# Kernel tuning notes

Measured on AMD Instinct MI355X. Metric: run time of the kernel, lower is better.

The kernel has to match this reference:

```python
import jax, jax.numpy as jnp
import numpy as np

HIDDEN = 100


def gcn_conv(x, W, b, src, dst, w, n):
    # GCNConv with symmetric normalization (self-loops already appended).
    xw = x @ W                                   # [N, H]
    deg = jax.ops.segment_sum(w, dst, num_segments=n)
    dinv = jnp.where(deg > 0, jax.lax.rsqrt(deg), 0.0)
    norm = dinv[src] * w * dinv[dst]             # [E]
    agg = jax.ops.segment_sum(norm[:, None] * xw[src], dst, num_segments=n)
    return agg + b


def setup_inputs() -> dict:
    key = jax.random.key(0)
    ks = jax.random.split(key, 16)
    N, F, E, H = 100000, 128, 1600000, HIDDEN
    x = jax.random.normal(ks[0], (N, F), dtype=jnp.float32)
    edge_index = jax.random.randint(ks[1], (2, E), 0, N, dtype=jnp.int64)
    edge_weight = jax.random.uniform(ks[2], (E,), dtype=jnp.float32)
    sF = 1.0 / np.sqrt(F)
    sH2 = 1.0 / np.sqrt(2 * H)
    sH = 1.0 / np.sqrt(H)
    inp = {
        "x": x, "edge_index": edge_index, "edge_weight": edge_weight,
        "Wcz": jax.random.normal(ks[3], (F, H), jnp.float32) * sF,
        "bcz": jnp.zeros((H,), jnp.float32),
        "Wcr": jax.random.normal(ks[4], (F, H), jnp.float32) * sF,
        "bcr": jnp.zeros((H,), jnp.float32),
        "Wch": jax.random.normal(ks[5], (F, H), jnp.float32) * sF,
        "bch": jnp.zeros((H,), jnp.float32),
        "Wlz": jax.random.normal(ks[6], (2 * H, H), jnp.float32) * sH2,
        "blz": jnp.zeros((H,), jnp.float32),
        "Wlr": jax.random.normal(ks[7], (2 * H, H), jnp.float32) * sH2,
        "blr": jnp.zeros((H,), jnp.float32),
        "Wlh": jax.random.normal(ks[8], (2 * H, H), jnp.float32) * sH2,
        "blh": jnp.zeros((H,), jnp.float32),
        "Wout": jax.random.normal(ks[9], (H, 1), jnp.float32) * sH,
        "bout": jnp.zeros((1,), jnp.float32),
    }
    return inp


def reference(x, edge_index, edge_weight,
              Wcz, bcz, Wcr, bcr, Wch, bch,
              Wlz, blz, Wlr, blr, Wlh, blh,
              Wout, bout):
    N = x.shape[0]
    # add self-loops with weight 1 (GCNConv default)
    loop = jnp.arange(N, dtype=edge_index.dtype)
    src = jnp.concatenate([edge_index[0], loop])
    dst = jnp.concatenate([edge_index[1], loop])
    w = jnp.concatenate([edge_weight, jnp.ones((N,), edge_weight.dtype)])

    H0 = jnp.zeros((N, HIDDEN), x.dtype)  # TGCN initial hidden state

    cz = gcn_conv(x, Wcz, bcz, src, dst, w, N)
    Z = jax.nn.sigmoid(jnp.concatenate([cz, H0], axis=1) @ Wlz + blz)

    cr = gcn_conv(x, Wcr, bcr, src, dst, w, N)
    R = jax.nn.sigmoid(jnp.concatenate([cr, H0], axis=1) @ Wlr + blr)

    ch = gcn_conv(x, Wch, bch, src, dst, w, N)
    Ht = jnp.tanh(jnp.concatenate([ch, H0 * R], axis=1) @ Wlh + blh)

    Hn = Z * H0 + (1.0 - Z) * Ht
    h = jax.nn.relu(Hn)
    return h @ Wout + bout
```

## Files before the change

kernel.cpp:

```cpp
#include <hip/hip_runtime.h>

#define FEAT 128
#define HID  100
#define CHUNK 2048

typedef __attribute__((ext_vector_type(8))) short short8;
typedef __attribute__((ext_vector_type(4))) float f32x4;

__device__ __forceinline__ unsigned short f2bf(float f) {
    union { float f; unsigned int u; } v; v.f = f;
    unsigned int r = v.u + 0x7fffu + ((v.u >> 16) & 1u);
    return (unsigned short)(r >> 16);
}

__device__ __forceinline__ int get_edge(const void* ei, int f64, long long pos) {
    return f64 ? (int)((const long long*)ei)[pos] : ((const int*)ei)[pos];
}

__device__ __forceinline__ int detect_f64(const void* ei) {
    const int* p = (const int*)ei;
    unsigned long long b = __ballot(p[2 * (threadIdx.x & 63) + 1] == 0);
    return b == ~0ull;
}

__global__ __launch_bounds__(256)
void k_front(const float* __restrict__ x, uint4* __restrict__ xb, int n8,
             const float* __restrict__ Wcz, const float* __restrict__ bcz,
             const float* __restrict__ Wch, const float* __restrict__ bch,
             const float* __restrict__ Wlz, const float* __restrict__ blz,
             const float* __restrict__ Wlh, const float* __restrict__ blh,
             const float* __restrict__ Wout,
             unsigned short* __restrict__ WB, float* __restrict__ bfold_ext,
             float* __restrict__ WoutZ,
             const void* ei, int* __restrict__ bucketCnt,
             int* __restrict__ blockBase, int NB, int E) {
    const int CVTB = 1024, FOLDB = 130;
    __shared__ int hist[1024];
    if (blockIdx.x < CVTB) {
        int stride = CVTB * 256;
        for (int i = blockIdx.x * 256 + threadIdx.x; i < n8; i += stride) {
            float4 a = *(const float4*)(x + (size_t)i * 8);
            float4 b = *(const float4*)(x + (size_t)i * 8 + 4);
            uint4 o;
            o.x = f2bf(a.x) | ((unsigned)f2bf(a.y) << 16);
            o.y = f2bf(a.z) | ((unsigned)f2bf(a.w) << 16);
            o.z = f2bf(b.x) | ((unsigned)f2bf(b.y) << 16);
            o.w = f2bf(b.z) | ((unsigned)f2bf(b.w) << 16);
            xb[i] = o;
        }
        return;
    }
    if (blockIdx.x < CVTB + FOLDB) {
        int idx = (blockIdx.x - CVTB) * 256 + threadIdx.x;
        if (idx < FEAT * 256) {
            int k = idx >> 8, n = idx & 255;
            float val = 0.f;
            if (n < HID) {
                for (int m = 0; m < HID; m++) val += Wcz[k * HID + m] * Wlz[m * HID + n];
            } else if (n >= 128 && n < 128 + HID) {
                int c = n - 128;
                for (int m = 0; m < HID; m++) val += Wch[k * HID + m] * Wlh[m * HID + c];
            }
            int ni = n >> 4, lc = n & 15, ks = k >> 5, hi = (k >> 3) & 3, j = k & 7;
            WB[(((ni * 4 + ks) * 64 + hi * 16 + lc) << 3) + j] = f2bf(val);
        } else if (idx < FEAT * 256 + 256) {
            int c = idx - FEAT * 256;
            float v = 0.f;
            if (c < HID) {
                v = blz[c];
                for (int j = 0; j < HID; j++) v += bcz[j] * Wlz[j * HID + c];
            } else if (c >= 128 && c < 128 + HID) {
                int cc = c - 128;
                v = blh[cc];
                for (int j = 0; j < HID; j++) v += bch[j] * Wlh[j * HID + cc];
            }
            bfold_ext[c] = v;
        } else if (idx < FEAT * 256 + 256 + 128) {
            int c = idx - FEAT * 256 - 256;
            WoutZ[c] = (c < HID) ? Wout[c] : 0.f;
        }
        return;
    }
    int f64 = detect_f64(ei);
    int cb = blockIdx.x - CVTB - FOLDB;
    int t = threadIdx.x;
    for (int i = t; i < NB; i += 256) hist[i] = 0;
    __syncthreads();
    int e0 = cb * CHUNK;
#pragma unroll
    for (int k = 0; k < CHUNK / 256; k++) {
        int e = e0 + k * 256 + t;
        if (e < E) {
            int d = get_edge(ei, f64, (long long)E + e);
            atomicAdd(&hist[d >> 8], 1);
        }
    }
    __syncthreads();
    int* bb = blockBase + (size_t)cb * NB;
    for (int b = t; b < NB; b += 256) {
        int c = hist[b];
        if (c) bb[b] = atomicAdd(&bucketCnt[b], c);
    }
}

__global__ void k_scanb(const int* __restrict__ bucketCnt, int* __restrict__ bucketStart,
                        int NB) {
    __shared__ int lds[1024];
    int t = threadIdx.x;
    int v = (t < NB) ? bucketCnt[t] : 0;
    lds[t] = v;
    __syncthreads();
    for (int off = 1; off < 1024; off <<= 1) {
        int tv = (t >= off) ? lds[t - off] : 0;
        __syncthreads();
        lds[t] += tv;
        __syncthreads();
    }
    if (t < NB) bucketStart[t] = lds[t] - v;
    if (t == NB - 1) bucketStart[NB] = lds[t];
}

__global__ __launch_bounds__(512)
void k_scatter(const void* ei, const float* __restrict__ w,
               const int* __restrict__ bucketStart, const int* __restrict__ blockBase,
               int2* __restrict__ sc, int NB, int E) {
    int f64 = detect_f64(ei);
    __shared__ int hist[1024];
    int t = threadIdx.x;
    for (int i = t; i < NB; i += 512) hist[i] = 0;
    __syncthreads();
    int e0 = blockIdx.x * CHUNK;
    const int* bb = blockBase + (size_t)blockIdx.x * NB;
    int sA[4], dA[4], wA[4], ok[4];
#pragma unroll
    for (int k = 0; k < 4; k++) {
        int e = e0 + k * 512 + t;
        ok[k] = (e < E);
        if (ok[k]) {
            sA[k] = get_edge(ei, f64, e);
            dA[k] = get_edge(ei, f64, (long long)E + e);
            wA[k] = __float_as_int(w[e]);
        }
    }
#pragma unroll
    for (int k = 0; k < 4; k++) {
        if (ok[k]) {
            int b = dA[k] >> 8;
            int r = atomicAdd(&hist[b], 1);
            int pos = bucketStart[b] + bb[b] + r;
            long long val = ((long long)wA[k] << 32)
                          | (unsigned)(sA[k] | ((dA[k] & 255) << 24));
            *(long long*)&sc[pos] = val;
        }
    }
}

__global__ __launch_bounds__(512)
void k_bucket(const int2* __restrict__ sc, const int* __restrict__ bucketStart,
              int* __restrict__ offs, int* __restrict__ cnt,
              int2* __restrict__ csr, float* __restrict__ dinv, int N) {
    __shared__ int hist[256];
    __shared__ int offsL[256];
    __shared__ int rank[256];
    __shared__ float wsum[256];
    int t = threadIdx.x;
    int n0 = blockIdx.x << 8;
    int s = bucketStart[blockIdx.x], e = bucketStart[blockIdx.x + 1];
    if (t < 256) { hist[t] = 0; rank[t] = 0; wsum[t] = 0.f; }
    __syncthreads();
    for (int i = s + t; i < e; i += 512)
        atomicAdd(&hist[((unsigned)sc[i].x) >> 24], 1);
    __syncthreads();
    int v = 0;
    if (t < 256) {
        v = (n0 + t < N) ? hist[t] + 1 : 0;
        offsL[t] = v;
    }
    __syncthreads();
    for (int off = 1; off < 256; off <<= 1) {
        int tv = (t < 256 && t >= off) ? offsL[t - off] : 0;
        __syncthreads();
        if (t < 256) offsL[t] += tv;
        __syncthreads();
    }
    int myOff = 0, myHist = 0;
    if (t < 256) { myOff = offsL[t] - v; myHist = hist[t]; }
    int csrBase = s + n0;
    if (t < 256 && n0 + t < N) {
        offs[n0 + t] = csrBase + myOff;
        cnt[n0 + t] = v;
    }
    __syncthreads();
    if (t < 256) offsL[t] = myOff;
    __syncthreads();
    for (int i = s + t; i < e; i += 512) {
        int2 en = sc[i];
        int dlow = ((unsigned)en.x) >> 24;
        int r = atomicAdd(&rank[dlow], 1);
        csr[csrBase + offsL[dlow] + r] = make_int2(en.x & 0xFFFFFF, en.y);
        atomicAdd(&wsum[dlow], __int_as_float(en.y));
    }
    __syncthreads();
    if (t < 256 && n0 + t < N) {
        dinv[n0 + t] = rsqrtf(1.f + wsum[t]);
        csr[csrBase + myOff + myHist] = make_int2(n0 + t, __float_as_int(1.0f));
    }
}

__global__ __launch_bounds__(256)
void k_agg4(const unsigned short* __restrict__ xb, const float* __restrict__ dinv,
            const int* __restrict__ offs, const int* __restrict__ cnt,
            const int2* __restrict__ csr, unsigned short* __restrict__ aggx,
            int nlo, int nhi) {
    int wid  = __builtin_amdgcn_readfirstlane(threadIdx.x >> 6);
    int lane = threadIdx.x & 63;
    long long node = (long long)nlo + blockIdx.x * 4 + wid;
    if (node >= nhi) return;
    int q  = lane >> 3;
    int fl = lane & 7;
    float acc[16];
#pragma unroll
    for (int j = 0; j < 16; j++) acc[j] = 0.f;
    int rs = offs[node];
    int c  = cnt[node];
    for (int i = q; i < c; i += 8) {
        int2 e = csr[rs + i];
        float nr = __int_as_float(e.y) * dinv[e.x];
        const uint4* xp = (const uint4*)(xb + (size_t)e.x * FEAT + fl * 16);
        uint4 v0 = xp[0];
        uint4 v1 = xp[1];
        const unsigned* u0 = &v0.x;
        const unsigned* u1 = &v1.x;
#pragma unroll
        for (int j = 0; j < 4; j++) {
            acc[2*j]         += nr * __uint_as_float(u0[j] << 16);
            acc[2*j + 1]     += nr * __uint_as_float(u0[j] & 0xffff0000u);
            acc[8 + 2*j]     += nr * __uint_as_float(u1[j] << 16);
            acc[8 + 2*j + 1] += nr * __uint_as_float(u1[j] & 0xffff0000u);
        }
    }
#pragma unroll
    for (int j = 0; j < 16; j++) {
        acc[j] += __shfl_xor(acc[j], 8);
        acc[j] += __shfl_xor(acc[j], 16);
        acc[j] += __shfl_xor(acc[j], 32);
    }
    if (q == 0) {
        float dn = dinv[node];
        uint4 o0, o1;
        unsigned* p0 = &o0.x;
        unsigned* p1 = &o1.x;
#pragma unroll
        for (int j = 0; j < 4; j++) {
            p0[j] = f2bf(acc[2*j] * dn)   | ((unsigned)f2bf(acc[2*j+1] * dn) << 16);
            p1[j] = f2bf(acc[8+2*j] * dn) | ((unsigned)f2bf(acc[8+2*j+1] * dn) << 16);
        }
        uint4* op = (uint4*)(aggx + (size_t)node * FEAT + fl * 16);
        op[0] = o0;
        op[1] = o1;
    }
}

__global__ __launch_bounds__(256)
void k_post3(const unsigned short* __restrict__ aggx, const unsigned short* __restrict__ WB,
             const float* __restrict__ bfold_ext, const float* __restrict__ WoutZ,
             const float* __restrict__ bout, float* __restrict__ out, int N) {
    __shared__ unsigned short At[64 * 136];
    __shared__ float red[64 * 4];
    int t = threadIdx.x;
    int lane = t & 63;
    int w = __builtin_amdgcn_readfirstlane(t >> 6);
    long long base = (long long)blockIdx.x * 64;

    for (int it = 0; it < 4; it++) {
        int idx = it * 256 + t;
        int row = idx >> 4, c16 = idx & 15;
        long long grow = base + row;
        uint4 v = make_uint4(0u, 0u, 0u, 0u);
        if (grow < N) v = *(const uint4*)(aggx + grow * FEAT + c16 * 8);
        *(uint4*)(At + row * 136 + c16 * 8) = v;
    }
    __syncthreads();

    int l15 = lane & 15, lhi = lane >> 4;
    int tadd = 2 * w;
    f32x4 acc[4][4];
#pragma unroll
    for (int ti = 0; ti < 4; ti++)
#pragma unroll
        for (int mi = 0; mi < 4; mi++) acc[ti][mi] = (f32x4)0.f;

    const int tiles[4] = {tadd, tadd + 1, tadd + 8, tadd + 9};
#pragma unroll
    for (int ks = 0; ks < 4; ks++) {
        short8 a[4];
#pragma unroll
        for (int mi = 0; mi < 4; mi++)
            a[mi] = *(const short8*)(At + (mi * 16 + l15) * 136 + ks * 32 + lhi * 8);
        short8 b[4];
#pragma unroll
        for (int ti = 0; ti < 4; ti++)
            b[ti] = *(const short8*)(WB + (((tiles[ti] * 4 + ks) * 64 + lane) << 3));
#pragma unroll
        for (int ti = 0; ti < 4; ti++)
#pragma unroll
            for (int mi = 0; mi < 4; mi++)
                acc[ti][mi] = __builtin_amdgcn_mfma_f32_16x16x32_bf16(
                    a[mi], b[ti], acc[ti][mi], 0, 0, 0);
    }

    float partial[4][4];
#pragma unroll
    for (int mi = 0; mi < 4; mi++)
#pragma unroll
        for (int r = 0; r < 4; r++) partial[mi][r] = 0.f;
#pragma unroll
    for (int d = 0; d < 2; d++) {
        int zcol = (tadd + d) * 16 + l15;
        float bz = bfold_ext[zcol];
        float bh = bfold_ext[zcol + 128];
        float wo = WoutZ[zcol];
#pragma unroll
        for (int mi = 0; mi < 4; mi++)
#pragma unroll
            for (int r = 0; r < 4; r++) {
                float az = acc[d][mi][r] + bz;
                float ah = acc[d + 2][mi][r] + bh;
                float z  = 1.f / (1.f + expf(-az));
                float ht = tanhf(ah);
                float h  = (1.f - z) * ht;
                h = h > 0.f ? h : 0.f;
                partial[mi][r] += h * wo;
            }
    }
#pragma unroll
    for (int mi = 0; mi < 4; mi++)
#pragma unroll
        for (int r = 0; r < 4; r++) {
            float p = partial[mi][r];
            p += __shfl_xor(p, 1);
            p += __shfl_xor(p, 2);
            p += __shfl_xor(p, 4);
            p += __shfl_xor(p, 8);
            partial[mi][r] = p;
        }
    if (l15 == 0) {
#pragma unroll
        for (int mi = 0; mi < 4; mi++)
#pragma unroll
            for (int r = 0; r < 4; r++)
                red[(mi * 16 + lhi * 4 + r) * 4 + w] = partial[mi][r];
    }
    __syncthreads();
    if (t < 64) {
        long long node = base + t;
        if (node < N)
            out[node] = red[t * 4] + red[t * 4 + 1] + red[t * 4 + 2] + red[t * 4 + 3]
                      + bout[0];
    }
}

extern "C" void kernel_launch(void* const* d_in, const int* in_sizes, int n_in,
                              void* d_out, int out_size, void* d_ws, size_t ws_size,
                              hipStream_t stream) {
    const float* x    = (const float*)d_in[0];
    const void*  ei   = d_in[1];
    const float* ew   = (const float*)d_in[2];
    const float* Wcz  = (const float*)d_in[3];
    const float* bcz  = (const float*)d_in[4];
    const float* Wch  = (const float*)d_in[7];
    const float* bch  = (const float*)d_in[8];
    const float* Wlz  = (const float*)d_in[9];
    const float* blz  = (const float*)d_in[10];
    const float* Wlh  = (const float*)d_in[13];
    const float* blh  = (const float*)d_in[14];
    const float* Wout = (const float*)d_in[15];
    const float* bout = (const float*)d_in[16];
    float* out = (float*)d_out;

    int N = in_sizes[0] / FEAT;
    int E = in_sizes[2];
    int NB = (N + 255) >> 8;
    int nblocksA = (E + CHUNK - 1) / CHUNK;

    char* p = (char*)d_ws;
    auto alloc = [&](size_t bytes) -> char* {
        char* r = p;
        p += (bytes + 255) & ~(size_t)255;
        return r;
    };
    float*          dinv        = (float*)alloc((size_t)N * 4);
    int*            cnt         = (int*)  alloc((size_t)N * 4);
    int*            offs        = (int*)  alloc((size_t)N * 4);
    int*            bucketCnt   = (int*)  alloc((size_t)(NB + 1) * 4);
    int*            bucketStart = (int*)  alloc((size_t)(NB + 1) * 4);
    int2*           csr         = (int2*) alloc((size_t)(E + N) * 8);
    unsigned short* xb          = (unsigned short*)alloc((size_t)N * FEAT * 2);
    unsigned short* aggx        = (unsigned short*)alloc((size_t)N * FEAT * 2);
    unsigned short* WB          = (unsigned short*)alloc((size_t)FEAT * 256 * 2);
    float*          bfold_ext   = (float*)alloc(256 * 4);
    float*          WoutZ       = (float*)alloc(128 * 4);
    int2* sc        = (int2*)aggx;
    int*  blockBase = (int*)((char*)aggx + (size_t)E * 8);

    hipMemsetAsync(bucketCnt, 0, (size_t)NB * 4, stream);
    k_front<<<1024 + 130 + nblocksA, 256, 0, stream>>>(
        x, (uint4*)xb, N * FEAT / 8,
        Wcz, bcz, Wch, bch, Wlz, blz, Wlh, blh, Wout, WB, bfold_ext, WoutZ,
        ei, bucketCnt, blockBase, NB, E);
    k_scanb<<<1, 1024, 0, stream>>>(bucketCnt, bucketStart, NB);
    k_scatter<<<nblocksA, 512, 0, stream>>>(ei, ew, bucketStart, blockBase, sc, NB, E);
    k_bucket<<<NB, 512, 0, stream>>>(sc, bucketStart, offs, cnt, csr, dinv, N);
    int Na = 33336, Nb2 = 66668;
    k_agg4<<<(Na + 3) / 4, 256, 0, stream>>>(xb, dinv, offs, cnt, csr, aggx, 0, Na);
    k_agg4<<<(Nb2 - Na + 3) / 4, 256, 0, stream>>>(xb, dinv, offs, cnt, csr, aggx, Na, Nb2);
    k_agg4<<<(N - Nb2 + 3) / 4, 256, 0, stream>>>(xb, dinv, offs, cnt, csr, aggx, Nb2, N);
    k_post3<<<(N + 63) / 64, 256, 0, stream>>>(aggx, WB, bfold_ext, WoutZ, bout, out, N);
}
```

Before: 295.8 us.

## Fuse bucket scan into scatter and bucket kernels, move x conversion, merge agg launches

New measurement: 284.9 us. 3.7% less time.

```diff
diff --git a/kernel.cpp b/kernel.cpp
--- a/kernel.cpp
+++ b/kernel.cpp
@@ -23,9 +23,27 @@
     return b == ~0ull;
 }
 
+__device__ __forceinline__ void scan_buckets(const int* __restrict__ bucketCnt,
+                                             int NB, int* bs) {
+    int t = threadIdx.x;
+    int v = (t < NB) ? bucketCnt[t] : 0;
+    if (t < NB) bs[t] = v;
+    __syncthreads();
+    for (int off = 1; off < NB; off <<= 1) {
+        int tv = (t < NB && t >= off) ? bs[t - off] : 0;
+        __syncthreads();
+        if (t < NB) bs[t] += tv;
+        __syncthreads();
+    }
+    int incl = (t < NB) ? bs[t] : 0;
+    __syncthreads();
+    if (t < NB) bs[t] = incl - v;
+    if (t == NB - 1) bs[NB] = incl;
+    __syncthreads();
+}
+
 __global__ __launch_bounds__(256)
-void k_front(const float* __restrict__ x, uint4* __restrict__ xb, int n8,
-             const float* __restrict__ Wcz, const float* __restrict__ bcz,
+void k_front(const float* __restrict__ Wcz, const float* __restrict__ bcz,
              const float* __restrict__ Wch, const float* __restrict__ bch,
              const float* __restrict__ Wlz, const float* __restrict__ blz,
              const float* __restrict__ Wlh, const float* __restrict__ blh,
@@ -34,24 +52,10 @@
              float* __restrict__ WoutZ,
              const void* ei, int* __restrict__ bucketCnt,
              int* __restrict__ blockBase, int NB, int E) {
-    const int CVTB = 1024, FOLDB = 130;
+    const int FOLDB = 130;
     __shared__ int hist[1024];
-    if (blockIdx.x < CVTB) {
-        int stride = CVTB * 256;
-        for (int i = blockIdx.x * 256 + threadIdx.x; i < n8; i += stride) {
-            float4 a = *(const float4*)(x + (size_t)i * 8);
-            float4 b = *(const float4*)(x + (size_t)i * 8 + 4);
-            uint4 o;
-            o.x = f2bf(a.x) | ((unsigned)f2bf(a.y) << 16);
-            o.y = f2bf(a.z) | ((unsigned)f2bf(a.w) << 16);
-            o.z = f2bf(b.x) | ((unsigned)f2bf(b.y) << 16);
-            o.w = f2bf(b.z) | ((unsigned)f2bf(b.w) << 16);
-            xb[i] = o;
-        }
-        return;
-    }
-    if (blockIdx.x < CVTB + FOLDB) {
-        int idx = (blockIdx.x - CVTB) * 256 + threadIdx.x;
+    if (blockIdx.x < FOLDB) {
+        int idx = blockIdx.x * 256 + threadIdx.x;
         if (idx < FEAT * 256) {
             int k = idx >> 8, n = idx & 255;
             float val = 0.f;
@@ -82,7 +86,7 @@
         return;
     }
     int f64 = detect_f64(ei);
-    int cb = blockIdx.x - CVTB - FOLDB;
+    int cb = blockIdx.x - FOLDB;
     int t = threadIdx.x;
     for (int i = t; i < NB; i += 256) hist[i] = 0;
     __syncthreads();
@@ -103,34 +107,36 @@
     }
 }
 
-__global__ void k_scanb(const int* __restrict__ bucketCnt, int* __restrict__ bucketStart,
-                        int NB) {
-    __shared__ int lds[1024];
+__global__ __launch_bounds__(512)
+void k_scvt(const float* __restrict__ x, uint4* __restrict__ xb, int n8,
+            const void* ei, const float* __restrict__ w,
+            const int* __restrict__ bucketCnt, const int* __restrict__ blockBase,
+            int2* __restrict__ sc, int NB, int E) {
+    const int CVTB = 1024;
+    __shared__ int hist[1024];
+    __shared__ int bs[1024];
+    if (blockIdx.x < CVTB) {
+        int stride = CVTB * 512;
+        for (int i = blockIdx.x * 512 + threadIdx.x; i < n8; i += stride) {
+            float4 a = *(const float4*)(x + (size_t)i * 8);
+            float4 b = *(const float4*)(x + (size_t)i * 8 + 4);
+            uint4 o;
+            o.x = f2bf(a.x) | ((unsigned)f2bf(a.y) << 16);
+            o.y = f2bf(a.z) | ((unsigned)f2bf(a.w) << 16);
+            o.z = f2bf(b.x) | ((unsigned)f2bf(b.y) << 16);
+            o.w = f2bf(b.z) | ((unsigned)f2bf(b.w) << 16);
+            xb[i] = o;
+        }
+        return;
+    }
+    int f64 = detect_f64(ei);
+    int cb = blockIdx.x - CVTB;
     int t = threadIdx.x;
-    int v = (t < NB) ? bucketCnt[t] : 0;
-    lds[t] = v;
-    __syncthreads();
-    for (int off = 1; off < 1024; off <<= 1) {
-        int tv = (t >= off) ? lds[t - off] : 0;
-        __syncthreads();
-        lds[t] += tv;
-        __syncthreads();
-    }
-    if (t < NB) bucketStart[t] = lds[t] - v;
-    if (t == NB - 1) bucketStart[NB] = lds[t];
-}
-
-__global__ __launch_bounds__(512)
-void k_scatter(const void* ei, const float* __restrict__ w,
-               const int* __restrict__ bucketStart, const int* __restrict__ blockBase,
-               int2* __restrict__ sc, int NB, int E) {
-    int f64 = detect_f64(ei);
-    __shared__ int hist[1024];
-    int t = threadIdx.x;
+    scan_buckets(bucketCnt, NB, bs);
     for (int i = t; i < NB; i += 512) hist[i] = 0;
     __syncthreads();
-    int e0 = blockIdx.x * CHUNK;
-    const int* bb = blockBase + (size_t)blockIdx.x * NB;
+    int e0 = cb * CHUNK;
+    const int* bb = blockBase + (size_t)cb * NB;
     int sA[4], dA[4], wA[4], ok[4];
 #pragma unroll
     for (int k = 0; k < 4; k++) {
@@ -147,7 +153,7 @@
         if (ok[k]) {
             int b = dA[k] >> 8;
             int r = atomicAdd(&hist[b], 1);
-            int pos = bucketStart[b] + bb[b] + r;
+            int pos = bs[b] + bb[b] + r;
             long long val = ((long long)wA[k] << 32)
                           | (unsigned)(sA[k] | ((dA[k] & 255) << 24));
             *(long long*)&sc[pos] = val;
@@ -156,16 +162,18 @@
 }
 
 __global__ __launch_bounds__(512)
-void k_bucket(const int2* __restrict__ sc, const int* __restrict__ bucketStart,
+void k_bucket(const int2* __restrict__ sc, const int* __restrict__ bucketCnt,
               int* __restrict__ offs, int* __restrict__ cnt,
-              int2* __restrict__ csr, float* __restrict__ dinv, int N) {
+              int2* __restrict__ csr, float* __restrict__ dinv, int N, int NB) {
+    __shared__ int bs[1024];
     __shared__ int hist[256];
     __shared__ int offsL[256];
     __shared__ int rank[256];
     __shared__ float wsum[256];
     int t = threadIdx.x;
+    scan_buckets(bucketCnt, NB, bs);
     int n0 = blockIdx.x << 8;
-    int s = bucketStart[blockIdx.x], e = bucketStart[blockIdx.x + 1];
+    int s = bs[blockIdx.x], e = bs[blockIdx.x + 1];
     if (t < 256) { hist[t] = 0; rank[t] = 0; wsum[t] = 0.f; }
     __syncthreads();
     for (int i = s + t; i < e; i += 512)
@@ -210,12 +218,11 @@
 __global__ __launch_bounds__(256)
 void k_agg4(const unsigned short* __restrict__ xb, const float* __restrict__ dinv,
             const int* __restrict__ offs, const int* __restrict__ cnt,
-            const int2* __restrict__ csr, unsigned short* __restrict__ aggx,
-            int nlo, int nhi) {
+            const int2* __restrict__ csr, unsigned short* __restrict__ aggx, int N) {
     int wid  = __builtin_amdgcn_readfirstlane(threadIdx.x >> 6);
     int lane = threadIdx.x & 63;
-    long long node = (long long)nlo + blockIdx.x * 4 + wid;
-    if (node >= nhi) return;
+    long long node = (long long)blockIdx.x * 4 + wid;
+    if (node >= N) return;
     int q  = lane >> 3;
     int fl = lane & 7;
     float acc[16];
@@ -393,7 +400,6 @@
     int*            cnt         = (int*)  alloc((size_t)N * 4);
     int*            offs        = (int*)  alloc((size_t)N * 4);
     int*            bucketCnt   = (int*)  alloc((size_t)(NB + 1) * 4);
-    int*            bucketStart = (int*)  alloc((size_t)(NB + 1) * 4);
     int2*           csr         = (int2*) alloc((size_t)(E + N) * 8);
     unsigned short* xb          = (unsigned short*)alloc((size_t)N * FEAT * 2);
     unsigned short* aggx        = (unsigned short*)alloc((size_t)N * FEAT * 2);
@@ -404,16 +410,12 @@
     int*  blockBase = (int*)((char*)aggx + (size_t)E * 8);
 
     hipMemsetAsync(bucketCnt, 0, (size_t)NB * 4, stream);
-    k_front<<<1024 + 130 + nblocksA, 256, 0, stream>>>(
-        x, (uint4*)xb, N * FEAT / 8,
+    k_front<<<130 + nblocksA, 256, 0, stream>>>(
         Wcz, bcz, Wch, bch, Wlz, blz, Wlh, blh, Wout, WB, bfold_ext, WoutZ,
         ei, bucketCnt, blockBase, NB, E);
-    k_scanb<<<1, 1024, 0, stream>>>(bucketCnt, bucketStart, NB);
-    k_scatter<<<nblocksA, 512, 0, stream>>>(ei, ew, bucketStart, blockBase, sc, NB, E);
-    k_bucket<<<NB, 512, 0, stream>>>(sc, bucketStart, offs, cnt, csr, dinv, N);
-    int Na = 33336, Nb2 = 66668;
-    k_agg4<<<(Na + 3) / 4, 256, 0, stream>>>(xb, dinv, offs, cnt, csr, aggx, 0, Na);
-    k_agg4<<<(Nb2 - Na + 3) / 4, 256, 0, stream>>>(xb, dinv, offs, cnt, csr, aggx, Na, Nb2);
-    k_agg4<<<(N - Nb2 + 3) / 4, 256, 0, stream>>>(xb, dinv, offs, cnt, csr, aggx, Nb2, N);
+    k_scvt<<<1024 + nblocksA, 512, 0, stream>>>(
+        x, (uint4*)xb, N * FEAT / 8, ei, ew, bucketCnt, blockBase, sc, NB, E);
+    k_bucket<<<NB, 512, 0, stream>>>(sc, bucketCnt, offs, cnt, csr, dinv, N, NB);
+    k_agg4<<<(N + 3) / 4, 256, 0, stream>>>(xb, dinv, offs, cnt, csr, aggx, N);
     k_post3<<<(N + 63) / 64, 256, 0, stream>>>(aggx, WB, bfold_ext, WoutZ, bout, out, N);
 }
```
